# Kernel optimization log

Hardware: AMD Instinct MI355X
Metric: run time of the kernel (lower is better)

The kernel has to match this reference:

```python
import jax, jax.numpy as jnp
import numpy as np

B, T, D = 32, 1024, 384
MAX_DUR = 4            # durations drawn from [0, MAX_DUR]
T_OUT = T * MAX_DUR    # fixed padded output length (upper bound on sum of durations)
PAD_VALUE = 0.0


def setup_inputs() -> dict:
    key = jax.random.key(0)
    k1, k2, k3 = jax.random.split(key, 3)
    xs = jax.random.normal(k1, (B, T, D), dtype=jnp.float32)
    durations = jax.random.randint(k2, (B, T), 0, MAX_DUR + 1).astype(jnp.int64)
    input_lengths = jax.random.randint(k3, (B,), 0, T).astype(jnp.int64)
    return {"xs": xs, "durations": durations, "input_lengths": input_lengths}


def reference(xs, durations, input_lengths):
    # Length regulator: repeat token t of sample b durations[b, t] times
    # (only for t < input_lengths[b]); pad expanded sequences with PAD_VALUE.
    # Vectorized via cumsum over durations + searchsorted gather.
    t_idx = jnp.arange(T)
    valid = t_idx[None, :] < input_lengths[:, None]            # [B, T]
    d = jnp.where(valid, durations, 0)                          # mask past input length
    total = d.sum(axis=-1)                                      # [B]
    # faithful to d.fill_(1) when all durations are zero
    d = jnp.where((total == 0)[:, None], valid.astype(d.dtype), d)
    total = d.sum(axis=-1)
    csum = jnp.cumsum(d, axis=-1)                               # [B, T] inclusive cumsum
    j = jnp.arange(T_OUT)
    # source token for output frame j: first t with csum[t] > j
    # (zero-duration tokens are skipped automatically by side='right')
    src = jax.vmap(lambda c: jnp.searchsorted(c, j, side='right'))(csum)  # [B, T_OUT]
    src = jnp.clip(src, 0, T - 1)
    out = jnp.take_along_axis(xs, src[:, :, None], axis=1)      # [B, T_OUT, D]
    out_mask = j[None, :] < total[:, None]                      # [B, T_OUT]
    return jnp.where(out_mask[:, :, None], out, jnp.asarray(PAD_VALUE, xs.dtype))
```

## Files before the change

kernel.cpp:

```cpp
#include <hip/hip_runtime.h>

#define BB 32
#define TT 1024
#define T_OUT 4096
#define DD 384
#define F4_PER_ROW (DD / 4)

typedef float f4 __attribute__((ext_vector_type(4)));

__global__ __launch_bounds__(256) void build_src_kernel(
    const int* __restrict__ durations,
    const int* __restrict__ input_lengths,
    int* __restrict__ src_idx) {
  const int b = blockIdx.x;
  const int tid = threadIdx.x;
  const int len = input_lengths[b];
  const int t0 = tid * 4;

  const int4 dv = *reinterpret_cast<const int4*>(&durations[b * TT + t0]);
  int d[4] = {dv.x, dv.y, dv.z, dv.w};
#pragma unroll
  for (int i = 0; i < 4; ++i)
    if (t0 + i >= len) d[i] = 0;

  int s = d[0] + d[1] + d[2] + d[3];

  const int lane = tid & 63;
  const int wid = tid >> 6;
  __shared__ int wred[4];
  __shared__ int wsum[4];
  int r = s;
#pragma unroll
  for (int off = 32; off > 0; off >>= 1) r += __shfl_xor(r, off);
  if (lane == 0) wred[wid] = r;
  __syncthreads();
  int total = wred[0] + wred[1] + wred[2] + wred[3];

  if (total == 0) {
#pragma unroll
    for (int i = 0; i < 4; ++i) d[i] = (t0 + i < len) ? 1 : 0;
    s = d[0] + d[1] + d[2] + d[3];
    total = len;
  }

  int v = s;
#pragma unroll
  for (int off = 1; off < 64; off <<= 1) {
    int u = __shfl_up(v, off);
    if (lane >= off) v += u;
  }
  if (lane == 63) wsum[wid] = v;
  __syncthreads();
  int wpre = 0;
#pragma unroll
  for (int w = 0; w < 4; ++w)
    if (w < wid) wpre += wsum[w];
  int run = wpre + v - s;

  int* base = src_idx + b * T_OUT;
#pragma unroll
  for (int i = 0; i < 4; ++i) {
    for (int k = 0; k < d[i]; ++k) base[run + k] = t0 + i;
    run += d[i];
  }

  for (int k = total + tid; k < T_OUT; k += 256) base[k] = -1;
}

#define G_BLOCKS 4096
#define G_ITERS 12
#define G_TILE (256 * G_ITERS)
static_assert((long long)G_BLOCKS * G_TILE == (long long)BB * T_OUT * F4_PER_ROW,
              "exact tiling");

__global__ __launch_bounds__(256) void gather_copy_kernel(
    const f4* __restrict__ xs,
    const int* __restrict__ src_idx,
    f4* __restrict__ out) {
  const unsigned base = blockIdx.x * (unsigned)G_TILE + threadIdx.x;
#pragma unroll
  for (int it = 0; it < G_ITERS; ++it) {
    const unsigned idx = base + (unsigned)it * 256u;
    const unsigned frame = idx / F4_PER_ROW;
    const unsigned lane = idx - frame * F4_PER_ROW;
    const int src = src_idx[frame];
    const unsigned b = frame >> 12;
    f4 val = {0.f, 0.f, 0.f, 0.f};
    if (src >= 0) {
      val = xs[((b << 10) + (unsigned)src) * F4_PER_ROW + lane];
    }
    out[idx] = val;
  }
}

extern "C" void kernel_launch(void* const* d_in, const int* in_sizes, int n_in,
                              void* d_out, int out_size, void* d_ws, size_t ws_size,
                              hipStream_t stream) {
  const float* xs = (const float*)d_in[0];
  const int* durations = (const int*)d_in[1];
  const int* input_lengths = (const int*)d_in[2];
  float* out = (float*)d_out;
  int* src_idx = (int*)d_ws;

  build_src_kernel<<<BB, 256, 0, stream>>>(durations, input_lengths, src_idx);

  gather_copy_kernel<<<G_BLOCKS, 256, 0, stream>>>(
      (const f4*)xs, src_idx, (f4*)out);
}
```

Baseline: 39.69 us.

## Fuse source-index build into gather kernel with per-block cumsum recompute

```diff
diff --git a/kernel.cpp b/kernel.cpp
--- a/kernel.cpp
+++ b/kernel.cpp
@@ -5,17 +5,29 @@
 #define T_OUT 4096
 #define DD 384
 #define F4_PER_ROW (DD / 4)
+#define FRAMES_PER_BLOCK 32
+#define BLOCKS_PER_BATCH (T_OUT / FRAMES_PER_BLOCK)
+#define G_ITERS (FRAMES_PER_BLOCK * F4_PER_ROW / 256)
 
 typedef float f4 __attribute__((ext_vector_type(4)));
 
-__global__ __launch_bounds__(256) void build_src_kernel(
+__global__ __launch_bounds__(256) void lenreg_fused_kernel(
+    const f4* __restrict__ xs,
     const int* __restrict__ durations,
     const int* __restrict__ input_lengths,
-    int* __restrict__ src_idx) {
-  const int b = blockIdx.x;
+    f4* __restrict__ out) {
+  const unsigned blk = blockIdx.x;
+  const unsigned b = blk / BLOCKS_PER_BATCH;
+  const unsigned f0 = (blk % BLOCKS_PER_BATCH) * FRAMES_PER_BLOCK;
   const int tid = threadIdx.x;
   const int len = input_lengths[b];
   const int t0 = tid * 4;
+
+  __shared__ int wred[4];
+  __shared__ int wsum[4];
+  __shared__ int map[FRAMES_PER_BLOCK];
+
+  if (tid < FRAMES_PER_BLOCK) map[tid] = -1;
 
   const int4 dv = *reinterpret_cast<const int4*>(&durations[b * TT + t0]);
   int d[4] = {dv.x, dv.y, dv.z, dv.w};
@@ -27,20 +39,17 @@
 
   const int lane = tid & 63;
   const int wid = tid >> 6;
-  __shared__ int wred[4];
-  __shared__ int wsum[4];
   int r = s;
 #pragma unroll
   for (int off = 32; off > 0; off >>= 1) r += __shfl_xor(r, off);
   if (lane == 0) wred[wid] = r;
   __syncthreads();
-  int total = wred[0] + wred[1] + wred[2] + wred[3];
+  const int total = wred[0] + wred[1] + wred[2] + wred[3];
 
   if (total == 0) {
 #pragma unroll
     for (int i = 0; i < 4; ++i) d[i] = (t0 + i < len) ? 1 : 0;
     s = d[0] + d[1] + d[2] + d[3];
-    total = len;
   }
 
   int v = s;
@@ -57,39 +66,28 @@
     if (w < wid) wpre += wsum[w];
   int run = wpre + v - s;
 
-  int* base = src_idx + b * T_OUT;
+  const int flo = (int)f0, fhi = (int)f0 + FRAMES_PER_BLOCK;
 #pragma unroll
   for (int i = 0; i < 4; ++i) {
-    for (int k = 0; k < d[i]; ++k) base[run + k] = t0 + i;
-    run += d[i];
+    int lo = run, hi = run + d[i];
+    run = hi;
+    lo = lo < flo ? flo : lo;
+    hi = hi > fhi ? fhi : hi;
+    for (int k = lo; k < hi; ++k) map[k - flo] = t0 + i;
   }
+  __syncthreads();
 
-  for (int k = total + tid; k < T_OUT; k += 256) base[k] = -1;
-}
-
-#define G_BLOCKS 4096
-#define G_ITERS 12
-#define G_TILE (256 * G_ITERS)
-static_assert((long long)G_BLOCKS * G_TILE == (long long)BB * T_OUT * F4_PER_ROW,
-              "exact tiling");
-
-__global__ __launch_bounds__(256) void gather_copy_kernel(
-    const f4* __restrict__ xs,
-    const int* __restrict__ src_idx,
-    f4* __restrict__ out) {
-  const unsigned base = blockIdx.x * (unsigned)G_TILE + threadIdx.x;
+  const f4* xrow = xs + (size_t)b * TT * F4_PER_ROW;
+  f4* obase = out + ((size_t)b * T_OUT + f0) * F4_PER_ROW;
 #pragma unroll
   for (int it = 0; it < G_ITERS; ++it) {
-    const unsigned idx = base + (unsigned)it * 256u;
-    const unsigned frame = idx / F4_PER_ROW;
-    const unsigned lane = idx - frame * F4_PER_ROW;
-    const int src = src_idx[frame];
-    const unsigned b = frame >> 12;
+    const unsigned o = (unsigned)it * 256u + (unsigned)tid;
+    const unsigned fl = o / F4_PER_ROW;
+    const unsigned ln = o - fl * F4_PER_ROW;
+    const int src = map[fl];
     f4 val = {0.f, 0.f, 0.f, 0.f};
-    if (src >= 0) {
-      val = xs[((b << 10) + (unsigned)src) * F4_PER_ROW + lane];
-    }
-    out[idx] = val;
+    if (src >= 0) val = xrow[(unsigned)src * F4_PER_ROW + ln];
+    obase[o] = val;
   }
 }
 
@@ -100,10 +98,7 @@
   const int* durations = (const int*)d_in[1];
   const int* input_lengths = (const int*)d_in[2];
   float* out = (float*)d_out;
-  int* src_idx = (int*)d_ws;
 
-  build_src_kernel<<<BB, 256, 0, stream>>>(durations, input_lengths, src_idx);
-
-  gather_copy_kernel<<<G_BLOCKS, 256, 0, stream>>>(
-      (const f4*)xs, src_idx, (f4*)out);
+  lenreg_fused_kernel<<<BB * BLOCKS_PER_BATCH, 256, 0, stream>>>(
+      (const f4*)xs, durations, input_lengths, (f4*)out);
 }
```

Result: faster. 35.28 us, median of 2 (-11.1%).
